# Optimization experiments

Measured on AMD Instinct MI355X. Metric: run time of the kernel, lower is better.

The kernel has to match this reference:

```python
import jax, jax.numpy as jnp
import numpy as np
import math

NPAD = 100      # npadding
NLAYERS = 4     # transformer_num_layers
NHEAD = 8       # transformer_nhead


def _posenc(T, d):
    pos = jnp.arange(T, dtype=jnp.float32)[:, None]
    div = jnp.exp(jnp.arange(0, d, 2, dtype=jnp.float32) * (-(math.log(1000.0) / d)))
    pe = jnp.zeros((T, d), jnp.float32)
    pe = pe.at[:, 0::2].set(jnp.sin(pos * div))
    pe = pe.at[:, 1::2].set(jnp.cos(pos * div))
    return pe


def _ln(x, g, b):
    m = x.mean(-1, keepdims=True)
    v = ((x - m) ** 2).mean(-1, keepdims=True)
    return (x - m) / jnp.sqrt(v + 1e-5) * g + b


def conv_individual(Y, kernel, npadding):
    # Y: (B,N,Ttot); kernel: (ntau,N). Causal zero-pad then FFT conv (faithful to source).
    B, N, Ttot = Y.shape
    kernel = jnp.concatenate([jnp.zeros((1, N), kernel.dtype), kernel], axis=0)
    ntau = kernel.shape[0]
    nn = Ttot + ntau - 1
    Yf = jnp.fft.fft(Y, n=nn, axis=2)                 # (B,N,nn) complex
    Kf = jnp.fft.fft(kernel.T, n=nn, axis=-1)          # (N,nn)
    c = jnp.fft.ifft(Yf * Kf[None], axis=2).real
    c = jnp.where(jnp.abs(c) < 1e-5, 0.0, c)           # ad-hoc small-value zeroing from source
    return c[:, :, :Ttot][:, :, npadding:]             # (B,N,T)


def conv_subspace(Y, kernel, npadding):
    # Y: (B,N,Ttot); kernel: (ntau,S) -> G: (B,N,S,T)
    B, N, Ttot = Y.shape
    k = kernel[None]                                   # (1,ntau,S)
    k = jnp.concatenate([jnp.zeros((1, 1, k.shape[2]), jnp.float32), k], axis=1)
    ntau = k.shape[1]
    nn = Ttot + ntau - 1
    Yf = jnp.fft.fft(Y, n=nn, axis=2)[..., None]       # (B,N,nn,1)
    Kf = jnp.fft.fft(k, n=nn, axis=1)[None]            # (1,1,nn,S)
    G = jnp.fft.ifft(Yf * Kf, axis=2).real             # (B,N,nn,S)
    G = jnp.where(jnp.abs(G) < 1e-5, 0.0, G)
    G = G[:, :, :Ttot, :][:, :, npadding:, :]
    return jnp.swapaxes(G, -1, -2)                     # (B,N,S,T)


def _encoder(x, Wqkv, bqkv, Wo, bo, ln1_g, ln1_b, W1, b1, W2, b2, ln2_g, ln2_b):
    B, T, D = x.shape
    hd = D // NHEAD
    for l in range(NLAYERS):
        qkv = x @ Wqkv[l] + bqkv[l]                    # (B,T,3D)
        q, k, v = jnp.split(qkv, 3, axis=-1)
        q = q.reshape(B, T, NHEAD, hd)
        k = k.reshape(B, T, NHEAD, hd)
        v = v.reshape(B, T, NHEAD, hd)
        scores = jnp.einsum('bthd,bshd->bhts', q, k) / jnp.sqrt(jnp.float32(hd))
        attn = jax.nn.softmax(scores, axis=-1)
        o = jnp.einsum('bhts,bshd->bthd', attn, v).reshape(B, T, D)
        x = _ln(x + (o @ Wo[l] + bo[l]), ln1_g[l], ln1_b[l])
        ff = jax.nn.gelu(x @ W1[l] + b1[l], approximate=False) @ W2[l] + b2[l]
        x = _ln(x + ff, ln2_g[l], ln2_b[l])
    return x


def reference(Y, token_W, token_b, Wqkv, bqkv, Wo, bo, ln1_g, ln1_b, W1, b1, W2, b2,
              ln2_g, ln2_b, toL_W, toL_b, dec_W1, dec_b1, dec_W2, dec_b2,
              stimulus_basis, readout_W, coupling_W, coupling_basis, self_kernel):
    B, N, Ttot = Y.shape
    T = Ttot - NPAD
    D = token_W.shape[1]
    # token conversion over time (seq dim = time)
    x = jnp.swapaxes(Y[:, :, NPAD:], 1, 2) @ token_W + token_b   # (B,T,D)
    x = x + _posenc(T, D)[None]
    x = _encoder(x, Wqkv, bqkv, Wo, bo, ln1_g, ln1_b, W1, b1, W2, b2, ln2_g, ln2_b)
    pooled = x.mean(axis=1)                                      # (B,D)
    h = pooled @ toL_W + toL_b                                   # (B,2Z)
    Z = h.shape[1] // 2
    z = h[:, :Z]                                                 # mu (sample_latent=False)
    # stimulus decoder (2-layer MLP)
    coeffs = jax.nn.relu(z @ dec_W1 + dec_b1) @ dec_W2 + dec_b2  # (B, NF*NB)
    NB = stimulus_basis.shape[1]
    NF = coeffs.shape[1] // NB
    coeffs = coeffs.reshape(B, NF, NB)
    sti_lat = jnp.einsum('bfk,tk->bft', coeffs, stimulus_basis)  # (B,NF,T)
    sti = jnp.einsum('nf,bft->bnt', readout_W, sti_lat)          # (B,N,T)
    # coupling via FFT causal conv into subspaces
    G = conv_subspace(Y, coupling_basis, NPAD)                   # (B,N,S,T)
    cpl = jnp.einsum('ns,bnst->bnt', coupling_W, G)
    # self-history FFT causal conv
    slf = conv_individual(Y, self_kernel, NPAD)
    return sti + cpl + slf                                       # log firing rate (B,N,T)


def setup_inputs() -> dict:
    key = jax.random.key(0)
    ks = jax.random.split(key, 30)
    B, N, Ttot = 16, 256, 1100
    D, FF, Zdim = 256, 1024, 64
    NB, NF, S, NTAU = 30, 4, 4, 20   # NF = narea*stimulus_nfactor = 2*2
    T = Ttot - NPAD
    sc = 0.02
    inp = {
        'Y': jax.random.uniform(ks[0], (B, N, Ttot), jnp.float32),
        'token_W': jax.random.normal(ks[1], (N, D), jnp.float32) * sc,
        'token_b': jnp.zeros((D,), jnp.float32),
        'Wqkv': jax.random.normal(ks[2], (NLAYERS, D, 3 * D), jnp.float32) * sc,
        'bqkv': jnp.zeros((NLAYERS, 3 * D), jnp.float32),
        'Wo': jax.random.normal(ks[3], (NLAYERS, D, D), jnp.float32) * sc,
        'bo': jnp.zeros((NLAYERS, D), jnp.float32),
        'ln1_g': jnp.ones((NLAYERS, D), jnp.float32),
        'ln1_b': jnp.zeros((NLAYERS, D), jnp.float32),
        'W1': jax.random.normal(ks[4], (NLAYERS, D, FF), jnp.float32) * sc,
        'b1': jnp.zeros((NLAYERS, FF), jnp.float32),
        'W2': jax.random.normal(ks[5], (NLAYERS, FF, D), jnp.float32) * sc,
        'b2': jnp.zeros((NLAYERS, D), jnp.float32),
        'ln2_g': jnp.ones((NLAYERS, D), jnp.float32),
        'ln2_b': jnp.zeros((NLAYERS, D), jnp.float32),
        'toL_W': jax.random.normal(ks[6], (D, 2 * Zdim), jnp.float32) * sc,
        'toL_b': jnp.zeros((2 * Zdim,), jnp.float32),
        'dec_W1': jax.random.normal(ks[7], (Zdim, 2 * Zdim), jnp.float32) * sc,
        'dec_b1': jnp.zeros((2 * Zdim,), jnp.float32),
        'dec_W2': jax.random.normal(ks[8], (2 * Zdim, NB * NF), jnp.float32) * sc * 0.001,
        'dec_b2': jnp.zeros((NB * NF,), jnp.float32),
        'stimulus_basis': jax.random.normal(ks[9], (T, NB), jnp.float32),
        'readout_W': jax.random.normal(ks[10], (N, NF), jnp.float32) * sc,
        'coupling_W': jax.random.normal(ks[11], (N, S), jnp.float32) * sc,
        'coupling_basis': jax.random.normal(ks[12], (NTAU, S), jnp.float32) * 0.1,
        'self_kernel': jax.random.normal(ks[13], (NTAU, N), jnp.float32) * 0.1,
    }
    return inp
```

## Files before the change

kernel.cpp:

```cpp
#include <hip/hip_runtime.h>
#include <math.h>

#define TT_   1000
#define TTOT_ 1100
#define NPAD_ 100
#define DD_   256
#define NN_   256

#define X_OFF    0u
#define XB_OFF   4096000u
#define O_OFF    6144000u
#define BIG_OFF  12288000u
#define WT_OFF   20480000u
#define PE_OFF   22085632u
#define PP_OFF   22341632u
#define PL_OFF   (PP_OFF + 32768u)
#define CF_OFF   (PL_OFF + 4096u)
#define CB_OFF   (CF_OFF + 1920u)
#define BQ_OFF   (CF_OFF + 1920u + 5120u)
#define STL_OFF  (BQ_OFF + 3072u)

#define SC2_ 0.25503902254649546f

typedef __attribute__((ext_vector_type(8))) short s16x8;
typedef __attribute__((ext_vector_type(4))) float f32x4;
typedef __attribute__((ext_vector_type(16))) float f32x16;
typedef __attribute__((ext_vector_type(4))) unsigned u32x4;

__device__ inline short f2bf(float f) {
    unsigned u = __float_as_uint(f);
    u += 0x7fffu + ((u >> 16) & 1u);
    return (short)(u >> 16);
}
__device__ inline float exp2i(float x) {
    float r; asm("v_exp_f32 %0, %1" : "=v"(r) : "v"(x)); return r;
}
__device__ inline float gelu_f(float v) {
    const float t = v * (0.7978845608f + 0.0356774081f * v * v);
    const float e = exp2i(t * 2.885390082f);
    const float th = 1.f - 2.f / (e + 1.f);
    return 0.5f * v * (1.f + th);
}

__device__ inline void gl_lds16(const short* g, short* l) {
    __builtin_amdgcn_global_load_lds(
        (const __attribute__((address_space(1))) void*)g,
        (__attribute__((address_space(3))) void*)l, 16, 0, 0);
}

__global__ __launch_bounds__(256) void wtr_k(const float* __restrict__ in,
                                             short* __restrict__ out, int K, int N,
                                             int qrows, float qs)
{
    __shared__ float t[32][33];
    const int n0 = blockIdx.x * 32, k0 = blockIdx.y * 32;
    in  += (size_t)blockIdx.z * K * N;
    out += (size_t)blockIdx.z * K * N;
    const int tx = threadIdx.x & 31, ty = threadIdx.x >> 5;
    #pragma unroll
    for (int i = 0; i < 4; ++i)
        t[ty + 8 * i][tx] = in[(size_t)(k0 + ty + 8 * i) * N + n0 + tx];
    __syncthreads();
    #pragma unroll
    for (int i = 0; i < 4; ++i) {
        const int row = n0 + ty + 8 * i;
        float f = t[tx][ty + 8 * i];
        if (row < qrows) f *= qs;
        out[(size_t)row * K + k0 + tx] = f2bf(f);
    }
}

__global__ __launch_bounds__(256) void ytr_k(const float* __restrict__ Y,
                                             short* __restrict__ out)
{
    __shared__ float t[32][33];
    const int b = blockIdx.z;
    const int t0 = blockIdx.x * 32, n0 = blockIdx.y * 32;
    const int tx = threadIdx.x & 31, ty = threadIdx.x >> 5;
    #pragma unroll
    for (int i = 0; i < 4; ++i) {
        const int tt = t0 + tx;
        t[ty + 8 * i][tx] = (tt < TT_)
            ? Y[((size_t)(b * NN_ + n0 + ty + 8 * i)) * TTOT_ + NPAD_ + tt] : 0.f;
    }
    __syncthreads();
    #pragma unroll
    for (int i = 0; i < 4; ++i) {
        const int tt = t0 + ty + 8 * i;
        if (tt < TT_)
            out[((size_t)(b * TT_ + tt)) * NN_ + n0 + tx] = f2bf(t[tx][ty + 8 * i]);
    }
}

__global__ void pe_k(float* __restrict__ PE)
{
    const int t = blockIdx.x, d = threadIdx.x;
    const float div = __expf(-(float)(d & ~1) * 0.0269834190585241f);
    const float ang = (float)t * div;
    PE[t * 256 + d] = (d & 1) ? cosf(ang) : sinf(ang);
}

__global__ void bscale_k(const float* __restrict__ in, float* __restrict__ out)
{
    const int i = blockIdx.x * 256 + threadIdx.x;
    if (i < 3072) {
        const int col = i % 768;
        out[i] = in[i] * ((col < 256) ? SC2_ : 1.f);
    }
}

template<int OUTBF, int ACT, int RES, int DUAL>
__global__ __launch_bounds__(256) void bgemm_k(const short* __restrict__ A,
                                               const short* __restrict__ Bt,
                                               const float* __restrict__ bias,
                                               const float* __restrict__ resid,
                                               void* __restrict__ Cout,
                                               short* __restrict__ Cb,
                                               int M, int N, int K, int nby)
{
    __shared__ short As[64 * 64];
    __shared__ short Bs[128 * 64];
    const int tid = threadIdx.x;

    const int nwg = gridDim.x;
    int gid = blockIdx.x;
    {
        const int q = nwg >> 3, r = nwg & 7;
        const int x = gid & 7, idx = gid >> 3;
        gid = (x < r ? x * (q + 1) : r * (q + 1) + (x - r) * q) + idx;
    }
    const int bx = gid / nby, by = gid - bx * nby;
    const int m0 = bx * 64, n0 = by * 128;

    const int wv = tid >> 6, lane = tid & 63;
    const int wr = wv >> 1, wc = wv & 1;
    const int l15 = lane & 15, lg = lane >> 4;

    f32x4 acc[2][4];
    #pragma unroll
    for (int i = 0; i < 2; ++i)
        #pragma unroll
        for (int j = 0; j < 4; ++j) acc[i][j] = (f32x4){0.f, 0.f, 0.f, 0.f};

    const int nt = K >> 6;
    for (int t = 0; t < nt; ++t) {
        __syncthreads();
        const int k0 = t << 6;
        #pragma unroll
        for (int i = 0; i < 2; ++i) {
            const int cid = i * 256 + tid;
            const int r = cid >> 3, c = cid & 7;
            gl_lds16(A + (size_t)(m0 + r) * K + k0 + ((c ^ (r & 7)) * 8), As + cid * 8);
        }
        #pragma unroll
        for (int i = 0; i < 4; ++i) {
            const int cid = i * 256 + tid;
            const int r = cid >> 3, c = cid & 7;
            gl_lds16(Bt + (size_t)(n0 + r) * K + k0 + ((c ^ (r & 7)) * 8), Bs + cid * 8);
        }
        __syncthreads();

        #pragma unroll
        for (int ks = 0; ks < 2; ++ks) {
            s16x8 af[2], bf[4];
            #pragma unroll
            for (int mi = 0; mi < 2; ++mi) {
                const int row = wr * 32 + mi * 16 + l15;
                const int ch = ks * 4 + lg;
                af[mi] = *(const s16x8*)(As + row * 64 + ((ch ^ (row & 7)) * 8));
            }
            #pragma unroll
            for (int ni = 0; ni < 4; ++ni) {
                const int col = wc * 64 + ni * 16 + l15;
                const int ch = ks * 4 + lg;
                bf[ni] = *(const s16x8*)(Bs + col * 64 + ((ch ^ (col & 7)) * 8));
            }
            #pragma unroll
            for (int mi = 0; mi < 2; ++mi)
                #pragma unroll
                for (int ni = 0; ni < 4; ++ni)
                    acc[mi][ni] = __builtin_amdgcn_mfma_f32_16x16x32_bf16(
                        af[mi], bf[ni], acc[mi][ni], 0, 0, 0);
        }
    }

    #pragma unroll
    for (int mi = 0; mi < 2; ++mi) {
        #pragma unroll
        for (int ni = 0; ni < 4; ++ni) {
            const int col = n0 + wc * 64 + ni * 16 + l15;
            const float bv = bias[col];
            #pragma unroll
            for (int r = 0; r < 4; ++r) {
                const int row = m0 + wr * 32 + mi * 16 + lg * 4 + r;
                float v = acc[mi][ni][r] + bv;
                if (RES == 1) v += resid[(size_t)row * N + col];
                if (RES == 2) v += resid[(size_t)(row % 1000) * N + col];
                if (ACT) v = 0.5f * v * (1.0f + erff(v * 0.70710678118654752f));
                if (OUTBF) ((short*)Cout)[(size_t)row * N + col] = f2bf(v);
                else       ((float*)Cout)[(size_t)row * N + col] = v;
                if (DUAL)  Cb[(size_t)row * N + col] = f2bf(v);
            }
        }
    }
}

template<int ACT>
__global__ __launch_bounds__(256) void bgemm_db_k(const short* __restrict__ A,
                                                  const short* __restrict__ Bt,
                                                  const float* __restrict__ bias,
                                                  short* __restrict__ Cout,
                                                  int M, int N, int K, int nby)
{
    __shared__ short SH[2 * 12288];
    const int tid = threadIdx.x;

    const int nwg = gridDim.x;
    int gid = blockIdx.x;
    {
        const int q = nwg >> 3, r = nwg & 7;
        const int x = gid & 7, idx = gid >> 3;
        gid = (x < r ? x * (q + 1) : r * (q + 1) + (x - r) * q) + idx;
    }
    const int bx = gid / nby, by = gid - bx * nby;
    const int m0 = bx * 64, n0 = by * 128;

    const int wv = tid >> 6, lane = tid & 63;
    const int wr = wv >> 1, wc = wv & 1;
    const int l15 = lane & 15, lg = lane >> 4;

    f32x4 acc[2][4];
    #pragma unroll
    for (int i = 0; i < 2; ++i)
        #pragma unroll
        for (int j = 0; j < 4; ++j) acc[i][j] = (f32x4){0.f, 0.f, 0.f, 0.f};

    auto STAGE = [&](int p, int k0) {
        short* dA = SH + p * 12288;
        short* dB = dA + 4096;
        #pragma unroll
        for (int i = 0; i < 2; ++i) {
            const int cid = i * 256 + tid;
            const int r = cid >> 3, c = cid & 7;
            gl_lds16(A + (size_t)(m0 + r) * K + k0 + ((c ^ (r & 7)) * 8), dA + cid * 8);
        }
        #pragma unroll
        for (int i = 0; i < 4; ++i) {
            const int cid = i * 256 + tid;
            const int r = cid >> 3, c = cid & 7;
            gl_lds16(Bt + (size_t)(n0 + r) * K + k0 + ((c ^ (r & 7)) * 8), dB + cid * 8);
        }
    };

    const int nt = K >> 6;
    STAGE(0, 0);
    int cur = 0;
    for (int t = 0; t < nt; ++t) {
        if (t + 1 < nt) {
            STAGE(cur ^ 1, (t + 1) << 6);
            asm volatile("s_waitcnt vmcnt(6)" ::: "memory");
        } else {
            asm volatile("s_waitcnt vmcnt(0)" ::: "memory");
        }
        __builtin_amdgcn_s_barrier();

        const short* Asb = SH + cur * 12288;
        const short* Bsb = Asb + 4096;
        #pragma unroll
        for (int ks = 0; ks < 2; ++ks) {
            s16x8 af[2], bf[4];
            #pragma unroll
            for (int mi = 0; mi < 2; ++mi) {
                const int row = wr * 32 + mi * 16 + l15;
                const int ch = ks * 4 + lg;
                af[mi] = *(const s16x8*)(Asb + row * 64 + ((ch ^ (row & 7)) * 8));
            }
            #pragma unroll
            for (int ni = 0; ni < 4; ++ni) {
                const int col = wc * 64 + ni * 16 + l15;
                const int ch = ks * 4 + lg;
                bf[ni] = *(const s16x8*)(Bsb + col * 64 + ((ch ^ (col & 7)) * 8));
            }
            #pragma unroll
            for (int mi = 0; mi < 2; ++mi)
                #pragma unroll
                for (int ni = 0; ni < 4; ++ni)
                    acc[mi][ni] = __builtin_amdgcn_mfma_f32_16x16x32_bf16(
                        af[mi], bf[ni], acc[mi][ni], 0, 0, 0);
        }
        asm volatile("s_waitcnt lgkmcnt(0)" ::: "memory");
        __builtin_amdgcn_s_barrier();
        cur ^= 1;
    }

    short* Cs = SH;
    #pragma unroll
    for (int mi = 0; mi < 2; ++mi)
        #pragma unroll
        for (int ni = 0; ni < 4; ++ni) {
            const int cl = wc * 64 + ni * 16 + l15;
            const float bv = bias[n0 + cl];
            #pragma unroll
            for (int r = 0; r < 4; ++r) {
                const int rl = wr * 32 + mi * 16 + lg * 4 + r;
                float v = acc[mi][ni][r] + bv;
                if (ACT) v = gelu_f(v);
                Cs[rl * 132 + cl] = f2bf(v);
            }
        }
    __syncthreads();
    #pragma unroll
    for (int i = 0; i < 4; ++i) {
        const int cid = i * 256 + tid;
        const int rl = cid >> 4, cc = (cid & 15) * 8;
        s16x8 vv = *(const s16x8*)(Cs + rl * 132 + cc);
        *(s16x8*)(Cout + (size_t)(m0 + rl) * N + n0 + cc) = vv;
    }
}

__global__ __launch_bounds__(512) void bgemmln_k(const short* __restrict__ A,
                                                 const short* __restrict__ Bt,
                                                 const float* __restrict__ bias,
                                                 const float* __restrict__ lng,
                                                 const float* __restrict__ lnb,
                                                 float* __restrict__ X,
                                                 short* __restrict__ Xb,
                                                 int K)
{
    __shared__ short As[32 * 64];
    __shared__ short Bs[256 * 64];
    __shared__ float red[32][4][2];
    __shared__ float mrs[32][2];
    const int tid = threadIdx.x;

    const int nwg = gridDim.x;
    int gid = blockIdx.x;
    {
        const int q = nwg >> 3, r = nwg & 7;
        const int x = gid & 7, idx = gid >> 3;
        gid = (x < r ? x * (q + 1) : r * (q + 1) + (x - r) * q) + idx;
    }
    const int m0 = gid * 32;

    const int wv = tid >> 6, lane = tid & 63;
    const int wr = wv >> 2, wcx = wv & 3;
    const int l15 = lane & 15, lg = lane >> 4;

    f32x4 acc[4];
    #pragma unroll
    for (int j = 0; j < 4; ++j) acc[j] = (f32x4){0.f, 0.f, 0.f, 0.f};

    const int nt = K >> 6;
    for (int t = 0; t < nt; ++t) {
        __syncthreads();
        const int k0 = t << 6;
        if (tid < 256) {
            const int r = tid >> 3, c = tid & 7;
            gl_lds16(A + (size_t)(m0 + r) * K + k0 + ((c ^ (r & 7)) * 8), As + tid * 8);
        }
        #pragma unroll
        for (int i = 0; i < 4; ++i) {
            const int cid = i * 512 + tid;
            const int r = cid >> 3, c = cid & 7;
            gl_lds16(Bt + (size_t)r * K + k0 + ((c ^ (r & 7)) * 8), Bs + cid * 8);
        }
        __syncthreads();

        #pragma unroll
        for (int ks = 0; ks < 2; ++ks) {
            s16x8 af, bf[4];
            {
                const int row = wr * 16 + l15;
                const int ch = ks * 4 + lg;
                af = *(const s16x8*)(As + row * 64 + ((ch ^ (row & 7)) * 8));
            }
            #pragma unroll
            for (int ni = 0; ni < 4; ++ni) {
                const int col = wcx * 64 + ni * 16 + l15;
                const int ch = ks * 4 + lg;
                bf[ni] = *(const s16x8*)(Bs + col * 64 + ((ch ^ (col & 7)) * 8));
            }
            #pragma unroll
            for (int ni = 0; ni < 4; ++ni)
                acc[ni] = __builtin_amdgcn_mfma_f32_16x16x32_bf16(af, bf[ni], acc[ni], 0, 0, 0);
        }
    }

    float v[4][4];
    #pragma unroll
    for (int ni = 0; ni < 4; ++ni) {
        const int col = wcx * 64 + ni * 16 + l15;
        const float bv = bias[col];
        #pragma unroll
        for (int r = 0; r < 4; ++r) {
            const int row = m0 + wr * 16 + lg * 4 + r;
            v[ni][r] = acc[ni][r] + bv + X[(size_t)row * 256 + col];
        }
    }

    #pragma unroll
    for (int r = 0; r < 4; ++r) {
        float ss = v[0][r] + v[1][r] + v[2][r] + v[3][r];
        float qq = v[0][r] * v[0][r] + v[1][r] * v[1][r]
                 + v[2][r] * v[2][r] + v[3][r] * v[3][r];
        #pragma unroll
        for (int msk = 1; msk < 16; msk <<= 1) {
            ss += __shfl_xor(ss, msk);
            qq += __shfl_xor(qq, msk);
        }
        if (l15 == 0) {
            const int rloc = wr * 16 + lg * 4 + r;
            red[rloc][wcx][0] = ss;
            red[rloc][wcx][1] = qq;
        }
    }
    __syncthreads();
    if (tid < 32) {
        const float s = red[tid][0][0] + red[tid][1][0] + red[tid][2][0] + red[tid][3][0];
        const float q = red[tid][0][1] + red[tid][1][1] + red[tid][2][1] + red[tid][3][1];
        const float mean = s * (1.f / 256.f);
        const float var = q * (1.f / 256.f) - mean * mean;
        mrs[tid][0] = mean;
        mrs[tid][1] = rsqrtf(var + 1e-5f);
    }
    __syncthreads();

    #pragma unroll
    for (int ni = 0; ni < 4; ++ni) {
        const int col = wcx * 64 + ni * 16 + l15;
        const float gg = lng[col], bb = lnb[col];
        #pragma unroll
        for (int r = 0; r < 4; ++r) {
            const int rloc = wr * 16 + lg * 4 + r;
            const int row = m0 + rloc;
            const float o = (v[ni][r] - mrs[rloc][0]) * mrs[rloc][1] * gg + bb;
            X[(size_t)row * 256 + col] = o;
            Xb[(size_t)row * 256 + col] = f2bf(o);
        }
    }
}

__global__ __launch_bounds__(512) void mattn_k(const short* __restrict__ qkv,
                                               short* __restrict__ o)
{
    int wg = blockIdx.x;
    wg = (wg & 7) * 64 + (wg >> 3);
    const int qt = wg & 3, h = (wg >> 2) & 7, b = wg >> 5;

    const int tid = threadIdx.x, wv = tid >> 6, lane = tid & 63;
    const int q31 = lane & 31, hi = lane >> 5;
    __shared__ short Ks[2][64 * 40];
    __shared__ short VT[2][32 * 72];

    const int q0w = qt * 256 + wv * 32;
    int qrow = q0w + q31; if (qrow > 999) qrow = 999;
    s16x8 bq[2];
    #pragma unroll
    for (int dh = 0; dh < 2; ++dh)
        bq[dh] = *(const s16x8*)(qkv + ((size_t)(b * TT_ + qrow)) * 768 + h * 32 + dh * 16 + hi * 8);

    f32x16 oacc;
    #pragma unroll
    for (int i = 0; i < 16; ++i) oacc[i] = 0.f;
    float lrun = 0.f;

    const int sr = tid >> 2, sc = tid & 3;
    const int u = tid & 255;
    const int kp = u >> 3, dq = (u & 7) * 4;
    s16x8 kreg;
    short4 va, vb;
    auto LOADT = [&](int kt) {
        if (tid < 256) {
            int t = kt * 64 + sr; if (t > 999) t = 999;
            kreg = *(const s16x8*)(qkv + ((size_t)(b * TT_ + t)) * 768 + 256 + h * 32 + sc * 8);
        } else {
            int t0 = kt * 64 + 2 * kp, t1 = t0 + 1;
            if (t0 > 999) t0 = 999;
            if (t1 > 999) t1 = 999;
            va = *(const short4*)(qkv + ((size_t)(b * TT_ + t0)) * 768 + 512 + h * 32 + dq);
            vb = *(const short4*)(qkv + ((size_t)(b * TT_ + t1)) * 768 + 512 + h * 32 + dq);
        }
    };
    auto WRITET = [&](int buf) {
        if (tid < 256) {
            *(s16x8*)(&Ks[buf][sr * 40 + sc * 8]) = kreg;
        } else {
            const int c = kp >> 2;
            const int ko = (2 * kp) & 7;
            const uint2 vaw = *(const uint2*)&va;
            const uint2 vbw = *(const uint2*)&vb;
            unsigned pk[4];
            pk[0] = __builtin_amdgcn_perm(vbw.x, vaw.x, 0x05040100u);
            pk[1] = __builtin_amdgcn_perm(vbw.x, vaw.x, 0x07060302u);
            pk[2] = __builtin_amdgcn_perm(vbw.y, vaw.y, 0x05040100u);
            pk[3] = __builtin_amdgcn_perm(vbw.y, vaw.y, 0x07060302u);
            #pragma unroll
            for (int j = 0; j < 4; ++j) {
                const int d = dq + j;
                *(unsigned*)(&VT[buf][d * 72 + ((c ^ (d >> 3)) * 8) + ko]) = pk[j];
            }
        }
    };

    LOADT(0); WRITET(0);
    __syncthreads();
    int cur = 0;

    for (int kt = 0; kt < 16; ++kt) {
        if (kt < 15) LOADT(kt + 1);

        f32x16 st[2];
        __builtin_amdgcn_s_setprio(1);
        #pragma unroll
        for (int kb = 0; kb < 2; ++kb) {
            s16x8 kf0 = *(const s16x8*)(&Ks[cur][(kb * 32 + q31) * 40 + hi * 8]);
            s16x8 kf1 = *(const s16x8*)(&Ks[cur][(kb * 32 + q31) * 40 + 16 + hi * 8]);
            f32x16 z;
            #pragma unroll
            for (int i = 0; i < 16; ++i) z[i] = 0.f;
            z = __builtin_amdgcn_mfma_f32_32x32x16_bf16(kf0, bq[0], z, 0, 0, 0);
            z = __builtin_amdgcn_mfma_f32_32x32x16_bf16(kf1, bq[1], z, 0, 0, 0);
            st[kb] = z;
        }
        __builtin_amdgcn_s_setprio(0);

        if (kt == 15) {
            #pragma unroll
            for (int kb = 0; kb < 2; ++kb)
                #pragma unroll
                for (int r = 0; r < 16; ++r) {
                    const int kloc = kb * 32 + (r & 3) + 8 * (r >> 2) + 4 * hi;
                    if (960 + kloc >= TT_) st[kb][r] = -1e30f;
                }
        }

        float sloc = 0.f;
        #pragma unroll
        for (int kb = 0; kb < 2; ++kb)
            #pragma unroll
            for (int r = 0; r < 16; ++r) {
                const float p = exp2i(st[kb][r]);
                st[kb][r] = p; sloc += p;
            }
        lrun += sloc;

        unsigned wk[2][4][2];
        #pragma unroll
        for (int kb = 0; kb < 2; ++kb)
            #pragma unroll
            for (int a = 0; a < 4; ++a)
                #pragma unroll
                for (int h2 = 0; h2 < 2; ++h2) {
                    unsigned rr;
                    asm("v_cvt_pk_bf16_f32 %0, %1, %2"
                        : "=v"(rr)
                        : "v"(st[kb][4 * a + 2 * h2]), "v"(st[kb][4 * a + 2 * h2 + 1]));
                    wk[kb][a][h2] = rr;
                }

        #pragma unroll
        for (int ks = 0; ks < 4; ++ks) {
            const int kb = ks >> 1, qq = ks & 1;
            unsigned X0 = wk[kb][2 * qq + 1][0], Y0 = wk[kb][2 * qq][0];
            unsigned X1 = wk[kb][2 * qq + 1][1], Y1 = wk[kb][2 * qq][1];
            asm("v_permlane32_swap_b32 %0, %1" : "+v"(X0), "+v"(Y0));
            asm("v_permlane32_swap_b32 %0, %1" : "+v"(X1), "+v"(Y1));
            u32x4 w4 = (u32x4){Y0, Y1, X0, X1};
            s16x8 pb = __builtin_bit_cast(s16x8, w4);
            s16x8 vf = *(const s16x8*)(&VT[cur][q31 * 72 + (((2 * ks + hi) ^ (q31 >> 3)) * 8)]);
            __builtin_amdgcn_s_setprio(1);
            oacc = __builtin_amdgcn_mfma_f32_32x32x16_bf16(vf, pb, oacc, 0, 0, 0);
            __builtin_amdgcn_s_setprio(0);
        }

        if (kt < 15) WRITET(cur ^ 1);
        __syncthreads();
        cur ^= 1;
    }

    lrun += __shfl_xor(lrun, 32);

    const int t = q0w + q31;
    if (t < TT_) {
        const float inv = 1.f / lrun;
        short* ob = o + ((size_t)(b * TT_ + t)) * 256 + h * 32;
        #pragma unroll
        for (int a = 0; a < 4; ++a) {
            unsigned w0, w1;
            asm("v_cvt_pk_bf16_f32 %0, %1, %2"
                : "=v"(w0) : "v"(oacc[4 * a + 0] * inv), "v"(oacc[4 * a + 1] * inv));
            asm("v_cvt_pk_bf16_f32 %0, %1, %2"
                : "=v"(w1) : "v"(oacc[4 * a + 2] * inv), "v"(oacc[4 * a + 3] * inv));
            const int d0 = 8 * a + 4 * hi;
            *(unsigned*)(ob + d0) = w0;
            *(unsigned*)(ob + d0 + 2) = w1;
        }
    }
}

__global__ __launch_bounds__(256) void pool_part_k(const float* __restrict__ X,
                                                   float* __restrict__ partial)
{
    const int b = blockIdx.x, seg = blockIdx.y, d = threadIdx.x;
    float s = 0.f;
    const int t0 = seg * 125;
    for (int t = t0; t < t0 + 125; ++t) s += X[((size_t)b * TT_ + t) * 256 + d];
    partial[(b * 8 + seg) * 256 + d] = s;
}
__global__ __launch_bounds__(256) void pool_red_k(const float* __restrict__ partial,
                                                  float* __restrict__ pooled)
{
    const int b = blockIdx.x, d = threadIdx.x;
    float s = 0.f;
    for (int k = 0; k < 8; ++k) s += partial[(b * 8 + k) * 256 + d];
    pooled[b * 256 + d] = s * (1.f / (float)TT_);
}

__global__ __launch_bounds__(128) void head_k(const float* __restrict__ pooled,
                                              const float* __restrict__ toLW,
                                              const float* __restrict__ toLb,
                                              const float* __restrict__ dW1,
                                              const float* __restrict__ db1,
                                              const float* __restrict__ dW2,
                                              const float* __restrict__ db2,
                                              float* __restrict__ coeffs)
{
    const int b = blockIdx.x, j = threadIdx.x;
    __shared__ float hs[64];
    __shared__ float hid[128];
    float a = toLb[j];
    for (int d = 0; d < 256; ++d) a += pooled[b * 256 + d] * toLW[d * 128 + j];
    if (j < 64) hs[j] = a;
    __syncthreads();
    float a2 = db1[j];
    for (int z = 0; z < 64; ++z) a2 += hs[z] * dW1[z * 128 + j];
    hid[j] = fmaxf(a2, 0.f);
    __syncthreads();
    if (j < 120) {
        float a3 = db2[j];
        for (int k = 0; k < 128; ++k) a3 += hid[k] * dW2[k * 120 + j];
        coeffs[b * 120 + j] = a3;
    }
}

__global__ void comb_k(const float* __restrict__ selfK,
                       const float* __restrict__ cplW,
                       const float* __restrict__ cplB,
                       float* __restrict__ comb)
{
    const int n = threadIdx.x;
    for (int ti = 0; ti < 20; ++ti) {
        float s = selfK[ti * 256 + n];
        #pragma unroll
        for (int si = 0; si < 4; ++si) s += cplW[n * 4 + si] * cplB[ti * 4 + si];
        comb[n * 20 + ti] = s;
    }
}

__global__ __launch_bounds__(256) void stilat_k(const float* __restrict__ SB,
                                                const float* __restrict__ coeffs,
                                                float* __restrict__ STL)
{
    const int bf = blockIdx.x;
    __shared__ float c[30];
    if (threadIdx.x < 30) c[threadIdx.x] = coeffs[(bf >> 2) * 120 + (bf & 3) * 30 + threadIdx.x];
    __syncthreads();
    for (int t = threadIdx.x; t < TT_; t += 256) {
        float acc = 0.f;
        const float* sp = SB + (size_t)t * 30;
        #pragma unroll
        for (int k = 0; k < 30; ++k) acc += c[k] * sp[k];
        STL[bf * TT_ + t] = acc;
    }
}

__global__ __launch_bounds__(256) void final_k(const float* __restrict__ Y,
                                               const float* __restrict__ STL,
                                               const float* __restrict__ roW,
                                               const float* __restrict__ comb,
                                               float* __restrict__ out)
{
    const int bx = blockIdx.x;
    const int ts = bx & 3, nc = (bx >> 2) & 31, b = bx >> 7;
    const int n0 = nc * 8, t0 = ts * 250;
    const int tid = threadIdx.x;
    __shared__ float rw[8][4], ck[8][20], yl[8][272];

    if (tid < 32) rw[tid >> 2][tid & 3] = roW[(n0 + (tid >> 2)) * 4 + (tid & 3)];
    if (tid >= 64 && tid < 224) {
        const int j = tid - 64;
        ck[j / 20][j % 20] = comb[(n0 + j / 20) * 20 + (j % 20)];
    }
    for (int j = tid; j < 2160; j += 256) {
        const int n = j / 270, jj = j - n * 270;
        yl[n][jj] = Y[((size_t)(b * 256 + n0 + n)) * TTOT_ + t0 + 80 + jj];
    }
    __syncthreads();

    if (tid < 250) {
        const int t = t0 + tid;
        float s4[4];
        #pragma unroll
        for (int f = 0; f < 4; ++f) s4[f] = STL[((size_t)b * 4 + f) * TT_ + t];
        #pragma unroll
        for (int n = 0; n < 8; ++n) {
            float acc = rw[n][0] * s4[0] + rw[n][1] * s4[1]
                      + rw[n][2] * s4[2] + rw[n][3] * s4[3];
            #pragma unroll
            for (int tau = 1; tau <= 20; ++tau)
                acc += ck[n][tau - 1] * yl[n][tid + 20 - tau];
            out[((size_t)(b * 256 + n0 + n)) * TT_ + t] = acc;
        }
    }
}

extern "C" void kernel_launch(void* const* d_in, const int* in_sizes, int n_in,
                              void* d_out, int out_size, void* d_ws, size_t ws_size,
                              hipStream_t stream)
{
    const float* Y      = (const float*)d_in[0];
    const float* tokW   = (const float*)d_in[1];
    const float* tokb   = (const float*)d_in[2];
    const float* Wqkv   = (const float*)d_in[3];
    const float* bqkv   = (const float*)d_in[4];
    const float* Wo     = (const float*)d_in[5];
    const float* bo     = (const float*)d_in[6];
    const float* ln1g   = (const float*)d_in[7];
    const float* ln1b   = (const float*)d_in[8];
    const float* W1     = (const float*)d_in[9];
    const float* b1     = (const float*)d_in[10];
    const float* W2     = (const float*)d_in[11];
    const float* b2     = (const float*)d_in[12];
    const float* ln2g   = (const float*)d_in[13];
    const float* ln2b   = (const float*)d_in[14];
    const float* toLW   = (const float*)d_in[15];
    const float* toLb   = (const float*)d_in[16];
    const float* dW1    = (const float*)d_in[17];
    const float* db1    = (const float*)d_in[18];
    const float* dW2    = (const float*)d_in[19];
    const float* db2    = (const float*)d_in[20];
    const float* SB     = (const float*)d_in[21];
    const float* roW    = (const float*)d_in[22];
    const float* cplW   = (const float*)d_in[23];
    const float* cplB   = (const float*)d_in[24];
    const float* selfK  = (const float*)d_in[25];

    float* ws  = (float*)d_ws;
    float* X   = ws + X_OFF;
    short* Xb  = (short*)(ws + XB_OFF);
    short* O   = (short*)(ws + O_OFF);
    short* BIG = (short*)(ws + BIG_OFF);
    short* WT  = (short*)(ws + WT_OFF);
    float* PE  = ws + PE_OFF;
    float* PP  = ws + PP_OFF;
    float* PL  = ws + PL_OFF;
    float* CF  = ws + CF_OFF;
    float* CB  = ws + CB_OFF;
    float* BQ  = ws + BQ_OFF;
    float* STL = ws + STL_OFF;

    short* WTqkv = WT;
    short* WTo   = WT + 786432;
    short* WTw1  = WT + 1048576;
    short* WTw2  = WT + 2097152;
    short* WTtok = WT + 3145728;
    short* Ybt   = BIG;

    wtr_k<<<dim3(24, 8, 4), 256, 0, stream>>>(Wqkv, WTqkv, 256, 768, 256, SC2_);
    wtr_k<<<dim3(8, 8, 4),  256, 0, stream>>>(Wo,   WTo,   256, 256, 0, 1.f);
    wtr_k<<<dim3(32, 8, 4), 256, 0, stream>>>(W1,   WTw1,  256, 1024, 0, 1.f);
    wtr_k<<<dim3(8, 32, 4), 256, 0, stream>>>(W2,   WTw2,  1024, 256, 0, 1.f);
    wtr_k<<<dim3(8, 8, 1),  256, 0, stream>>>(tokW, WTtok, 256, 256, 0, 1.f);
    bscale_k<<<12, 256, 0, stream>>>(bqkv, BQ);
    pe_k<<<1000, 256, 0, stream>>>(PE);
    ytr_k<<<dim3(32, 8, 16), 256, 0, stream>>>(Y, Ybt);

    bgemm_k<0, 0, 2, 1><<<500, 256, 0, stream>>>(
        Ybt, WTtok, tokb, PE, X, Xb, 16000, 256, 256, 2);

    for (int l = 0; l < 4; ++l) {
        bgemm_db_k<0><<<1500, 256, 0, stream>>>(
            Xb, WTqkv + (size_t)l * 196608, BQ + l * 768, BIG,
            16000, 768, 256, 6);
        mattn_k<<<512, 512, 0, stream>>>(BIG, O);
        bgemmln_k<<<500, 512, 0, stream>>>(
            O, WTo + (size_t)l * 65536, bo + l * 256,
            ln1g + l * 256, ln1b + l * 256, X, Xb, 256);
        bgemm_db_k<1><<<2000, 256, 0, stream>>>(
            Xb, WTw1 + (size_t)l * 262144, b1 + l * 1024, BIG,
            16000, 1024, 256, 8);
        bgemmln_k<<<500, 512, 0, stream>>>(
            BIG, WTw2 + (size_t)l * 262144, b2 + l * 256,
            ln2g + l * 256, ln2b + l * 256, X, Xb, 1024);
    }

    pool_part_k<<<dim3(16, 8), 256, 0, stream>>>(X, PP);
    pool_red_k<<<16, 256, 0, stream>>>(PP, PL);
    head_k<<<16, 128, 0, stream>>>(PL, toLW, toLb, dW1, db1, dW2, db2, CF);
    comb_k<<<1, 256, 0, stream>>>(selfK, cplW, cplB, CB);
    stilat_k<<<64, 256, 0, stream>>>(SB, CF, STL);
    final_k<<<2048, 256, 0, stream>>>(Y, STL, roW, CB, (float*)d_out);
}
```

Before: 494.8 us.

## Fuse FFN W1+GELU+W2+residual+LayerNorm into one kernel keeping hidden in LDS

```diff
diff --git a/kernel.cpp b/kernel.cpp
--- a/kernel.cpp
+++ b/kernel.cpp
@@ -315,6 +315,158 @@
         const int rl = cid >> 4, cc = (cid & 15) * 8;
         s16x8 vv = *(const s16x8*)(Cs + rl * 132 + cc);
         *(s16x8*)(Cout + (size_t)(m0 + rl) * N + n0 + cc) = vv;
+    }
+}
+
+__global__ __launch_bounds__(512) void ffused_k(const short* __restrict__ A,
+                                                const short* __restrict__ W1t,
+                                                const float* __restrict__ b1,
+                                                const short* __restrict__ W2t,
+                                                const float* __restrict__ b2,
+                                                const float* __restrict__ lng,
+                                                const float* __restrict__ lnb,
+                                                float* __restrict__ X,
+                                                short* __restrict__ Xbo)
+{
+    __shared__ short As[32 * 256];
+    __shared__ short Ws[64 * 256];
+    __shared__ short Hs[32 * 512];
+    const int tid = threadIdx.x;
+
+    const int nwg = gridDim.x;
+    int gid = blockIdx.x;
+    {
+        const int q = nwg >> 3, r = nwg & 7;
+        const int x = gid & 7, idx = gid >> 3;
+        gid = (x < r ? x * (q + 1) : r * (q + 1) + (x - r) * q) + idx;
+    }
+    const int m0 = gid * 32;
+
+    const int wv = tid >> 6, lane = tid & 63;
+    const int wr = wv >> 2, wcq = wv & 3;
+    const int l15 = lane & 15, lg = lane >> 4;
+
+    #pragma unroll
+    for (int i = 0; i < 2; ++i) {
+        const int cid = i * 512 + tid;
+        const int r = cid >> 5, c = cid & 31;
+        gl_lds16(A + (size_t)(m0 + r) * 256 + ((c ^ (r & 7)) * 8), As + cid * 8);
+    }
+
+    f32x4 acc2[4];
+    #pragma unroll
+    for (int j = 0; j < 4; ++j) acc2[j] = (f32x4){0.f, 0.f, 0.f, 0.f};
+
+    for (int h = 0; h < 2; ++h) {
+        for (int nc = 0; nc < 8; ++nc) {
+            const int ng = h * 512 + nc * 64;
+            __syncthreads();
+            #pragma unroll
+            for (int i = 0; i < 4; ++i) {
+                const int cid = i * 512 + tid;
+                const int r = cid >> 5, c = cid & 31;
+                gl_lds16(W1t + (size_t)(ng + r) * 256 + ((c ^ (r & 7)) * 8), Ws + cid * 8);
+            }
+            __syncthreads();
+
+            f32x4 a1 = (f32x4){0.f, 0.f, 0.f, 0.f};
+            #pragma unroll
+            for (int ks = 0; ks < 8; ++ks) {
+                const int row = wr * 16 + l15;
+                const int ch = ks * 4 + lg;
+                s16x8 af = *(const s16x8*)(As + row * 256 + ((ch ^ (row & 7)) * 8));
+                const int col = wcq * 16 + l15;
+                s16x8 bf = *(const s16x8*)(Ws + col * 256 + ((ch ^ (col & 7)) * 8));
+                a1 = __builtin_amdgcn_mfma_f32_16x16x32_bf16(af, bf, a1, 0, 0, 0);
+            }
+            const int col = wcq * 16 + l15;
+            const float bv = b1[ng + col];
+            const int hc = nc * 64 + col;
+            #pragma unroll
+            for (int r2 = 0; r2 < 4; ++r2) {
+                const int row = wr * 16 + lg * 4 + r2;
+                Hs[row * 512 + (hc ^ ((row & 7) << 3))] = f2bf(gelu_f(a1[r2] + bv));
+            }
+        }
+        for (int kc = 0; kc < 8; ++kc) {
+            __syncthreads();
+            const int koff = h * 512 + kc * 64;
+            #pragma unroll
+            for (int i = 0; i < 4; ++i) {
+                const int cid = i * 512 + tid;
+                const int r = cid >> 3, c = cid & 7;
+                gl_lds16(W2t + (size_t)r * 1024 + koff + ((c ^ (r & 7)) * 8), Ws + cid * 8);
+            }
+            __syncthreads();
+            #pragma unroll
+            for (int ks = 0; ks < 2; ++ks) {
+                const int row = wr * 16 + l15;
+                const int ch = kc * 8 + ks * 4 + lg;
+                s16x8 af = *(const s16x8*)(Hs + row * 512 + ((ch ^ (row & 7)) * 8));
+                #pragma unroll
+                for (int ni = 0; ni < 4; ++ni) {
+                    const int n = wcq * 64 + ni * 16 + l15;
+                    s16x8 bf = *(const s16x8*)(Ws + n * 64 + (((ks * 4 + lg) ^ (n & 7)) * 8));
+                    acc2[ni] = __builtin_amdgcn_mfma_f32_16x16x32_bf16(af, bf, acc2[ni], 0, 0, 0);
+                }
+            }
+        }
+    }
+
+    __syncthreads();
+    float* redf = (float*)Ws;
+    float* mrsf = redf + 256;
+
+    float v[4][4];
+    #pragma unroll
+    for (int ni = 0; ni < 4; ++ni) {
+        const int col = wcq * 64 + ni * 16 + l15;
+        const float bv = b2[col];
+        #pragma unroll
+        for (int r = 0; r < 4; ++r) {
+            const int row = m0 + wr * 16 + lg * 4 + r;
+            v[ni][r] = acc2[ni][r] + bv + X[(size_t)row * 256 + col];
+        }
+    }
+    #pragma unroll
+    for (int r = 0; r < 4; ++r) {
+        float ss = v[0][r] + v[1][r] + v[2][r] + v[3][r];
+        float qq = v[0][r] * v[0][r] + v[1][r] * v[1][r]
+                 + v[2][r] * v[2][r] + v[3][r] * v[3][r];
+        #pragma unroll
+        for (int msk = 1; msk < 16; msk <<= 1) {
+            ss += __shfl_xor(ss, msk);
+            qq += __shfl_xor(qq, msk);
+        }
+        if (l15 == 0) {
+            const int rl = wr * 16 + lg * 4 + r;
+            redf[(rl * 4 + wcq) * 2 + 0] = ss;
+            redf[(rl * 4 + wcq) * 2 + 1] = qq;
+        }
+    }
+    __syncthreads();
+    if (tid < 32) {
+        float s = 0.f, q = 0.f;
+        #pragma unroll
+        for (int w = 0; w < 4; ++w) { s += redf[(tid * 4 + w) * 2]; q += redf[(tid * 4 + w) * 2 + 1]; }
+        const float mean = s * (1.f / 256.f);
+        const float var = q * (1.f / 256.f) - mean * mean;
+        mrsf[tid * 2 + 0] = mean;
+        mrsf[tid * 2 + 1] = rsqrtf(var + 1e-5f);
+    }
+    __syncthreads();
+    #pragma unroll
+    for (int ni = 0; ni < 4; ++ni) {
+        const int col = wcq * 64 + ni * 16 + l15;
+        const float gg = lng[col], bb = lnb[col];
+        #pragma unroll
+        for (int r = 0; r < 4; ++r) {
+            const int rl = wr * 16 + lg * 4 + r;
+            const int row = m0 + rl;
+            const float o = (v[ni][r] - mrsf[rl * 2]) * mrsf[rl * 2 + 1] * gg + bb;
+            X[(size_t)row * 256 + col] = o;
+            Xbo[(size_t)row * 256 + col] = f2bf(o);
+        }
     }
 }
 
@@ -786,12 +938,10 @@
         bgemmln_k<<<500, 512, 0, stream>>>(
             O, WTo + (size_t)l * 65536, bo + l * 256,
             ln1g + l * 256, ln1b + l * 256, X, Xb, 256);
-        bgemm_db_k<1><<<2000, 256, 0, stream>>>(
-            Xb, WTw1 + (size_t)l * 262144, b1 + l * 1024, BIG,
-            16000, 1024, 256, 8);
-        bgemmln_k<<<500, 512, 0, stream>>>(
-            BIG, WTw2 + (size_t)l * 262144, b2 + l * 256,
-            ln2g + l * 256, ln2b + l * 256, X, Xb, 1024);
+        ffused_k<<<500, 512, 0, stream>>>(
+            Xb, WTw1 + (size_t)l * 262144, b1 + l * 1024,
+            WTw2 + (size_t)l * 262144, b2 + l * 256,
+            ln2g + l * 256, ln2b + l * 256, X, Xb);
     }
 
     pool_part_k<<<dim3(16, 8), 256, 0, stream>>>(X, PP);
```

New measurement: 498.4 us. About the same (+0.7%).
